# Kernel tuning notes

Measured on AMD Instinct MI355X. Metric: run time of the kernel, lower is better.

## Reference

```python
import jax, jax.numpy as jnp
import numpy as np

N, E = 20000, 160000
F, H, OUT = 256, 8, 128
L = 6            # total layers -> 5 GAT layers
LM1 = L - 1
NGN = L // 3 + 1 # 3 GraphNorms
D = F // H       # 32 per head
GN_FREQ = 3
EPS = 1e-5


def setup_inputs() -> dict:
    key = jax.random.key(0)
    ks = jax.random.split(key, 12)
    x = jax.random.normal(ks[0], (N, 1), dtype=jnp.float32)
    edge_index = jax.random.randint(ks[1], (2, E), 0, N, dtype=jnp.int32)
    W0 = jax.random.normal(ks[2], (1, F), dtype=jnp.float32) * 0.1
    b0 = jnp.zeros((F,), jnp.float32)
    gat_lin = jax.random.normal(ks[3], (LM1, F, F), dtype=jnp.float32) * (1.0 / np.sqrt(F))
    att_src = jax.random.normal(ks[4], (LM1, H, D), dtype=jnp.float32) * 0.1
    att_dst = jax.random.normal(ks[5], (LM1, H, D), dtype=jnp.float32) * 0.1
    gat_bias = jnp.zeros((LM1, F), jnp.float32)
    gn_weight = jnp.ones((NGN, F), jnp.float32)
    gn_bias = jnp.zeros((NGN, F), jnp.float32)
    gn_mean_scale = jnp.ones((NGN, F), jnp.float32)
    lin_W = jax.random.normal(ks[6], (F, OUT), dtype=jnp.float32) * (1.0 / np.sqrt(F))
    lin_b = jnp.zeros((OUT,), jnp.float32)
    return {"x": x, "W0": W0, "b0": b0, "gat_lin": gat_lin, "att_src": att_src,
            "att_dst": att_dst, "gat_bias": gat_bias, "gn_weight": gn_weight,
            "gn_bias": gn_bias, "gn_mean_scale": gn_mean_scale,
            "lin_W": lin_W, "lin_b": lin_b, "edge_index": edge_index}


def _gcn_conv(x, W, b, src, dst, n):
    h = x @ W
    deg = jax.ops.segment_sum(jnp.ones(src.shape[0], h.dtype), dst, num_segments=n)
    dinv = jnp.where(deg > 0, jax.lax.rsqrt(deg), 0.0)
    norm = dinv[src] * dinv[dst]                      # [E']
    out = jax.ops.segment_sum(h[src] * norm[:, None], dst, num_segments=n)
    return out + b


def _gat_conv(x, W, a_src, a_dst, src, dst, n):
    # PyG GATConv (concat=True, negative_slope=0.2, self-loops in src/dst)
    h = (x @ W).reshape(n, H, D)
    s = jnp.einsum('nhd,hd->nh', h, a_src)            # [N,H]
    t = jnp.einsum('nhd,hd->nh', h, a_dst)
    e = jax.nn.leaky_relu(s[src] + t[dst], 0.2)       # [E',H]
    m = jax.ops.segment_max(e, dst, num_segments=n)   # per-dst softmax
    e = jnp.exp(e - m[dst])
    denom = jax.ops.segment_sum(e, dst, num_segments=n)
    alpha = e / (denom[dst] + 1e-16)
    out = jax.ops.segment_sum(h[src] * alpha[:, :, None], dst, num_segments=n)
    return out.reshape(n, F)


def _graph_norm(x, w, b, ms):
    # PyG GraphNorm with batch=None (single graph): per-feature stats over nodes
    mean = jnp.mean(x, axis=0)
    out = x - ms * mean
    var = jnp.mean(out * out, axis=0)
    return w * out * jax.lax.rsqrt(var + EPS) + b


def reference(x, W0, b0, gat_lin, att_src, att_dst, gat_bias, gn_weight, gn_bias,
              gn_mean_scale, lin_W, lin_b, edge_index):
    n = x.shape[0]
    loops = jnp.arange(n, dtype=edge_index.dtype)
    src = jnp.concatenate([edge_index[0], loops])
    dst = jnp.concatenate([edge_index[1], loops])
    h = jax.nn.relu(_gcn_conv(x, W0, b0, src, dst, n))
    for i in range(LM1):
        if i % GN_FREQ == 0:
            g = i // GN_FREQ
            h = _graph_norm(h, gn_weight[g], gn_bias[g], gn_mean_scale[g])
        out = _gat_conv(h, gat_lin[i], att_src[i], att_dst[i], src, dst, n)
        if i % GN_FREQ == 0:
            out = out + gat_bias[i]
        h = h + jax.nn.relu(out)
    return h @ lin_W + lin_b
```

## Files before the change

kernel.cpp:

```cpp
#include <hip/hip_runtime.h>
#include <hip/hip_bf16.h>
#include <stdint.h>

typedef float f32x4 __attribute__((ext_vector_type(4)));
typedef short s16x8 __attribute__((ext_vector_type(8)));

__device__ __forceinline__ float bf2f(unsigned short u) {
    union { unsigned int i; float f; } v; v.i = ((unsigned int)u) << 16; return v.f;
}
__device__ __forceinline__ unsigned short f2bf(float f) {
    union { float f; unsigned int i; } v; v.f = f;
    unsigned int x = v.i;
    return (unsigned short)((x + 0x7fffu + ((x >> 16) & 1u)) >> 16);
}
__device__ __forceinline__ void bfp(unsigned int u, float& lo, float& hi) {
    union { unsigned int i; float f; } a, b;
    a.i = u << 16; b.i = u & 0xffff0000u;
    lo = a.f; hi = b.f;
}
__device__ __forceinline__ void gload16(const void* g, void* l) {
    __builtin_amdgcn_global_load_lds(
        (const __attribute__((address_space(1))) void*)g,
        (__attribute__((address_space(3))) void*)l, 16, 0, 0);
}

__global__ void k_prep(const int* __restrict__ ei, int E, int* __restrict__ deg,
                       int CB,
                       const float* __restrict__ gat_lin,
                       const float* __restrict__ lin_W,
                       const float* __restrict__ att_src,
                       const float* __restrict__ att_dst,
                       unsigned short* __restrict__ Wt,
                       unsigned short* __restrict__ lt) {
    int bid = blockIdx.x;
    if (bid < CB) {
        int e = bid * 256 + threadIdx.x;
        if (e < E) atomicAdd(&deg[ei[E + e]], 1);
        return;
    }
    int idx = (bid - CB) * 256 + threadIdx.x;
    const int T1 = 5 * 65536;
    const int T2 = T1 + 128 * 256;
    const int T3 = T2 + 5 * 64 * 256;
    if (idx < T1) {
        int l = idx >> 16, r = idx & 0xFFFF;
        int nrow = r >> 8, k = r & 255;
        Wt[(size_t)l * 81920 + nrow * 256 + k] =
            f2bf(gat_lin[(size_t)l * 65536 + k * 256 + nrow]);
    } else if (idx < T2) {
        int j = idx - T1;
        int nrow = j >> 8, k = j & 255;
        lt[nrow * 256 + k] = f2bf(lin_W[(size_t)k * 128 + nrow]);
    } else if (idx < T3) {
        int j = idx - T2;
        int l = j >> 14, r = j & 16383;
        int row = r >> 8, k = r & 255;
        float v = 0.f;
        if (row < 16) {
            int head = row & 7;
            const float* a = (row < 8) ? (att_src + l * 256 + head * 32)
                                       : (att_dst + l * 256 + head * 32);
            const float* wr = gat_lin + (size_t)l * 65536 + k * 256 + head * 32;
#pragma unroll
            for (int d = 0; d < 32; ++d) v += wr[d] * a[d];
        }
        Wt[(size_t)l * 81920 + (256 + row) * 256 + k] = f2bf(v);
    }
}

__global__ __launch_bounds__(256) void k_bsum(const int* __restrict__ deg,
                                              int* __restrict__ bsum, int n) {
    __shared__ int buf[256];
    int i = blockIdx.x * 256 + threadIdx.x;
    buf[threadIdx.x] = (i < n) ? deg[i] + 1 : 0;
    __syncthreads();
#pragma unroll
    for (int off = 128; off > 0; off >>= 1) {
        if ((int)threadIdx.x < off) buf[threadIdx.x] += buf[threadIdx.x + off];
        __syncthreads();
    }
    if (threadIdx.x == 0) bsum[blockIdx.x] = buf[0];
}

__global__ __launch_bounds__(256) void k_emit(const int* __restrict__ deg,
                                              const int* __restrict__ bsum,
                                              int* __restrict__ rowptr,
                                              int* __restrict__ wo,
                                              float* __restrict__ dinv, int n) {
    __shared__ int buf[256];
    int t = threadIdx.x;
    int bid = blockIdx.x;
    buf[t] = (t < bid) ? bsum[t] : 0;
    __syncthreads();
#pragma unroll
    for (int off = 128; off > 0; off >>= 1) {
        if (t < off) buf[t] += buf[t + off];
        __syncthreads();
    }
    int boff = buf[0];
    __syncthreads();
    int i = bid * 256 + t;
    int v = (i < n) ? deg[i] + 1 : 0;
    buf[t] = v;
    __syncthreads();
    for (int off = 1; off < 256; off <<= 1) {
        int add = (t >= off) ? buf[t - off] : 0;
        __syncthreads();
        buf[t] += add;
        __syncthreads();
    }
    if (i < n) {
        int excl = boff + buf[t] - v;
        rowptr[i] = excl;
        wo[i] = excl;
        dinv[i] = rsqrtf((float)v);
        if (i == n - 1) rowptr[n] = excl + v;
    }
}

__global__ void k_fill(const int* __restrict__ ei, int E, int n,
                       int* wo, int* srcs) {
    int e = blockIdx.x * blockDim.x + threadIdx.x;
    int EP = E + n;
    if (e >= EP) return;
    int s_, d_;
    if (e < E) { s_ = ei[e]; d_ = ei[E + e]; }
    else       { s_ = d_ = e - E; }
    int pos = atomicAdd(&wo[d_], 1);
    srcs[pos] = s_;
}

__global__ __launch_bounds__(256) void k_h0f(const float* __restrict__ x,
                                             const float* __restrict__ dinv,
                                             const int* __restrict__ rowptr,
                                             const int* __restrict__ srcs,
                                             const float* __restrict__ W0,
                                             const float* __restrict__ b0,
                                             unsigned short* __restrict__ hbf,
                                             int n, int Mpad) {
    int wave = threadIdx.x >> 6, lane = threadIdx.x & 63;
    int node = blockIdx.x * 4 + wave;
    if (node >= Mpad) return;
    size_t base = (size_t)node * 256 + lane * 4;
    if (node >= n) {
        ushort4 z = {0, 0, 0, 0};
        *reinterpret_cast<ushort4*>(hbf + base) = z;
        return;
    }
    int p0 = rowptr[node], p1 = rowptr[node + 1];
    float sum = 0.f;
    for (int p = p0 + lane; p < p1; p += 64) {
        int s = srcs[p];
        sum += x[s] * dinv[s];
    }
#pragma unroll
    for (int m = 1; m < 64; m <<= 1) sum += __shfl_xor(sum, m);
    float sv = sum * dinv[node];
    float4 wv = *reinterpret_cast<const float4*>(W0 + lane * 4);
    float4 bv = *reinterpret_cast<const float4*>(b0 + lane * 4);
    ushort4 o;
    o.x = f2bf(fmaxf(sv * wv.x + bv.x, 0.f));
    o.y = f2bf(fmaxf(sv * wv.y + bv.y, 0.f));
    o.z = f2bf(fmaxf(sv * wv.z + bv.z, 0.f));
    o.w = f2bf(fmaxf(sv * wv.w + bv.w, 0.f));
    *reinterpret_cast<ushort4*>(hbf + base) = o;
}

__global__ __launch_bounds__(256) void k_gn_reduce(const unsigned short* __restrict__ hbf,
                                                   float* sums, float* sumsq, int n) {
    int f = threadIdx.x;
    float s = 0.f, q = 0.f;
    for (int r = blockIdx.x; r < n; r += gridDim.x) {
        float v = bf2f(hbf[(size_t)r * 256 + f]);
        s += v; q += v * v;
    }
    atomicAdd(&sums[f], s);
    atomicAdd(&sumsq[f], q);
}

__global__ __launch_bounds__(256) void k_gnfold(const float* __restrict__ st,
                                                const float* __restrict__ w,
                                                const float* __restrict__ b,
                                                const float* __restrict__ ms,
                                                unsigned short* __restrict__ Wt,
                                                float* __restrict__ so,
                                                float* __restrict__ rowbias,
                                                float ninv) {
    __shared__ float red[256];
    int col = blockIdx.x, k = threadIdx.x;
    float mean = st[k] * ninv;
    float m2   = st[256 + k] * ninv;
    float msf  = ms[k];
    float var  = m2 + msf * mean * mean * (msf - 2.0f);
    float sc = w[k] * rsqrtf(var + 1e-5f);
    float of = b[k] - msf * mean * sc;
    size_t idx = (size_t)col * 256 + k;
    float wv = bf2f(Wt[idx]);
    red[k] = of * wv;
    __syncthreads();
#pragma unroll
    for (int off = 128; off > 0; off >>= 1) {
        if (k < off) red[k] += red[k + off];
        __syncthreads();
    }
    if (k == 0) rowbias[col] = red[0];
    Wt[idx] = f2bf(sc * wv);
    if (col == 0) { so[k] = sc; so[256 + k] = of; }
}

#define BM 64
__global__ __launch_bounds__(512) void k_gemm_mfma(
    const unsigned short* __restrict__ A,
    const unsigned short* __restrict__ Bt,
    unsigned short* __restrict__ Cb,
    float* __restrict__ Cf,
    float* __restrict__ sbuf,
    float* __restrict__ tbuf,
    const float* __restrict__ bias,
    const float* __restrict__ rowbias,
    int M, int ldc)
{
    __shared__ unsigned short As[64 * 256];
    __shared__ unsigned short Bs[64 * 256];
    const int tid = threadIdx.x;
    const int bm = blockIdx.x * BM;
    const int bn = blockIdx.y * 64;
    {
        const char* ga = (const char*)(A + (size_t)bm * 256);
        const char* gb = (const char*)(Bt + (size_t)bn * 256);
        char* la = (char*)As;
        char* lb = (char*)Bs;
#pragma unroll
        for (int i = 0; i < 4; ++i) {
            int o  = (i * 512 + tid) * 16;
            int so = o ^ (((o >> 9) & 7) << 4);
            gload16(ga + so, la + o);
            gload16(gb + so, lb + o);
        }
    }
    __syncthreads();

    const int lane = tid & 63;
    const int w  = tid >> 6;
    const int wm = (w >> 1) * 16;
    const int wn = (w & 1) * 32;
    const int r  = lane & 15, kb = lane >> 4;
    const int r4 = (lane >> 4) * 4, cc = lane & 15;
    const char* la = (const char*)As;
    const char* lb = (const char*)Bs;

    f32x4 acc[2] = {};
#pragma unroll
    for (int ks = 0; ks < 8; ++ks) {
        int row = wm + r;
        int c16 = (ks * 4 + kb) ^ (row & 7);
        s16x8 af = *(const s16x8*)(la + row * 512 + c16 * 16);
#pragma unroll
        for (int j = 0; j < 2; ++j) {
            int col = wn + j * 16 + r;
            int d16 = (ks * 4 + kb) ^ (col & 7);
            s16x8 bfr = *(const s16x8*)(lb + col * 512 + d16 * 16);
            acc[j] = __builtin_amdgcn_mfma_f32_16x16x32_bf16(af, bfr, acc[j], 0, 0, 0);
        }
    }
#pragma unroll
    for (int j = 0; j < 2; ++j) {
        int col = bn + wn + j * 16 + cc;
        float rb = rowbias ? rowbias[col] : 0.f;
#pragma unroll
        for (int q = 0; q < 4; ++q) {
            int row = bm + wm + r4 + q;
            float v = acc[j][q] + rb;
            if (Cb) {
                if (col < 256) {
                    Cb[(size_t)row * 256 + col] = f2bf(v);
                } else if (col < 264) {
                    sbuf[(size_t)row * 8 + (col - 256)] = v;
                } else if (col < 272) {
                    tbuf[(size_t)row * 8 + (col - 264)] = v;
                }
            } else if (row < M) {
                Cf[(size_t)row * ldc + col] = v + bias[col];
            }
        }
    }
}

__global__ __launch_bounds__(256) void k_fagg(const unsigned short* __restrict__ h1,
                                              const float* __restrict__ sbuf,
                                              const float* __restrict__ tbuf,
                                              const int* __restrict__ rowptr,
                                              const int* __restrict__ srcs,
                                              unsigned short* __restrict__ hbf,
                                              const float* __restrict__ bias,
                                              const float* __restrict__ so, int n) {
    int wave = threadIdx.x >> 6, lane = threadIdx.x & 63;
    int node = blockIdx.x * 4 + wave;
    if (node >= n) return;
    int p0 = rowptr[node], p1 = rowptr[node + 1];
    int hid = lane >> 5;
    int l5 = lane & 31;
    int fl = l5 * 8;
    int head = l5 >> 2;
    float tv = tbuf[node * 8 + head];
    float m = -1e30f, den = 0.f;
    float a0 = 0.f, a1 = 0.f, a2 = 0.f, a3 = 0.f;
    float a4 = 0.f, a5 = 0.f, a6 = 0.f, a7 = 0.f;
    int q = p0 + hid;
    for (; q + 6 < p1; q += 8) {
        int s0 = srcs[q], s1 = srcs[q + 2], s2 = srcs[q + 4], s3 = srcs[q + 6];
        float e0 = sbuf[s0 * 8 + head] + tv;
        float e1 = sbuf[s1 * 8 + head] + tv;
        float e2 = sbuf[s2 * 8 + head] + tv;
        float e3 = sbuf[s3 * 8 + head] + tv;
        uint4 v0 = *reinterpret_cast<const uint4*>(h1 + (size_t)s0 * 256 + fl);
        uint4 v1 = *reinterpret_cast<const uint4*>(h1 + (size_t)s1 * 256 + fl);
        uint4 v2 = *reinterpret_cast<const uint4*>(h1 + (size_t)s2 * 256 + fl);
        uint4 v3 = *reinterpret_cast<const uint4*>(h1 + (size_t)s3 * 256 + fl);
        e0 = (e0 > 0.f) ? e0 : 0.2f * e0;
        e1 = (e1 > 0.f) ? e1 : 0.2f * e1;
        e2 = (e2 > 0.f) ? e2 : 0.2f * e2;
        e3 = (e3 > 0.f) ? e3 : 0.2f * e3;
        float em = fmaxf(fmaxf(e0, e1), fmaxf(e2, e3));
        if (em > m + 8.f) {
            float sc = __expf(m - em);
            den *= sc;
            a0 *= sc; a1 *= sc; a2 *= sc; a3 *= sc;
            a4 *= sc; a5 *= sc; a6 *= sc; a7 *= sc;
            m = em;
        }
        float w0 = __expf(e0 - m), w1 = __expf(e1 - m);
        float w2 = __expf(e2 - m), w3 = __expf(e3 - m);
        den += (w0 + w1) + (w2 + w3);
        float fl0, fh0, fl1, fh1, fl2, fh2, fl3, fh3;
        bfp(v0.x, fl0, fh0); bfp(v1.x, fl1, fh1); bfp(v2.x, fl2, fh2); bfp(v3.x, fl3, fh3);
        a0 += (w0 * fl0 + w1 * fl1) + (w2 * fl2 + w3 * fl3);
        a1 += (w0 * fh0 + w1 * fh1) + (w2 * fh2 + w3 * fh3);
        bfp(v0.y, fl0, fh0); bfp(v1.y, fl1, fh1); bfp(v2.y, fl2, fh2); bfp(v3.y, fl3, fh3);
        a2 += (w0 * fl0 + w1 * fl1) + (w2 * fl2 + w3 * fl3);
        a3 += (w0 * fh0 + w1 * fh1) + (w2 * fh2 + w3 * fh3);
        bfp(v0.z, fl0, fh0); bfp(v1.z, fl1, fh1); bfp(v2.z, fl2, fh2); bfp(v3.z, fl3, fh3);
        a4 += (w0 * fl0 + w1 * fl1) + (w2 * fl2 + w3 * fl3);
        a5 += (w0 * fh0 + w1 * fh1) + (w2 * fh2 + w3 * fh3);
        bfp(v0.w, fl0, fh0); bfp(v1.w, fl1, fh1); bfp(v2.w, fl2, fh2); bfp(v3.w, fl3, fh3);
        a6 += (w0 * fl0 + w1 * fl1) + (w2 * fl2 + w3 * fl3);
        a7 += (w0 * fh0 + w1 * fh1) + (w2 * fh2 + w3 * fh3);
    }
    for (; q < p1; q += 2) {
        int s0 = srcs[q];
        float e0 = sbuf[s0 * 8 + head] + tv;
        uint4 v0 = *reinterpret_cast<const uint4*>(h1 + (size_t)s0 * 256 + fl);
        e0 = (e0 > 0.f) ? e0 : 0.2f * e0;
        if (e0 > m + 8.f) {
            float sc = __expf(m - e0);
            den *= sc;
            a0 *= sc; a1 *= sc; a2 *= sc; a3 *= sc;
            a4 *= sc; a5 *= sc; a6 *= sc; a7 *= sc;
            m = e0;
        }
        float w0 = __expf(e0 - m);
        den += w0;
        float f0l, f0h;
        bfp(v0.x, f0l, f0h); a0 += w0 * f0l; a1 += w0 * f0h;
        bfp(v0.y, f0l, f0h); a2 += w0 * f0l; a3 += w0 * f0h;
        bfp(v0.z, f0l, f0h); a4 += w0 * f0l; a5 += w0 * f0h;
        bfp(v0.w, f0l, f0h); a6 += w0 * f0l; a7 += w0 * f0h;
    }
    float mo = __shfl_xor(m, 32);
    float mm = fmaxf(m, mo);
    float sc = __expf(m - mm);
    den *= sc; den += __shfl_xor(den, 32);
    a0 *= sc; a0 += __shfl_xor(a0, 32);
    a1 *= sc; a1 += __shfl_xor(a1, 32);
    a2 *= sc; a2 += __shfl_xor(a2, 32);
    a3 *= sc; a3 += __shfl_xor(a3, 32);
    a4 *= sc; a4 += __shfl_xor(a4, 32);
    a5 *= sc; a5 += __shfl_xor(a5, 32);
    a6 *= sc; a6 += __shfl_xor(a6, 32);
    a7 *= sc; a7 += __shfl_xor(a7, 32);
    if (hid) return;
    float inv = 1.0f / (den + 1e-16f);
    a0 *= inv; a1 *= inv; a2 *= inv; a3 *= inv;
    a4 *= inv; a5 *= inv; a6 *= inv; a7 *= inv;
    float b_[8] = {0.f, 0.f, 0.f, 0.f, 0.f, 0.f, 0.f, 0.f};
    if (bias) {
        float4 blo = *reinterpret_cast<const float4*>(bias + fl);
        float4 bhi = *reinterpret_cast<const float4*>(bias + fl + 4);
        b_[0] = blo.x; b_[1] = blo.y; b_[2] = blo.z; b_[3] = blo.w;
        b_[4] = bhi.x; b_[5] = bhi.y; b_[6] = bhi.z; b_[7] = bhi.w;
    }
    size_t base = (size_t)node * 256 + fl;
    uint4 hv = *reinterpret_cast<const uint4*>(hbf + base);
    float h_[8];
    bfp(hv.x, h_[0], h_[1]); bfp(hv.y, h_[2], h_[3]);
    bfp(hv.z, h_[4], h_[5]); bfp(hv.w, h_[6], h_[7]);
    if (so) {
        float4 s0v = *reinterpret_cast<const float4*>(so + fl);
        float4 s1v = *reinterpret_cast<const float4*>(so + fl + 4);
        float4 o0v = *reinterpret_cast<const float4*>(so + 256 + fl);
        float4 o1v = *reinterpret_cast<const float4*>(so + 256 + fl + 4);
        h_[0] = h_[0] * s0v.x + o0v.x; h_[1] = h_[1] * s0v.y + o0v.y;
        h_[2] = h_[2] * s0v.z + o0v.z; h_[3] = h_[3] * s0v.w + o0v.w;
        h_[4] = h_[4] * s1v.x + o1v.x; h_[5] = h_[5] * s1v.y + o1v.y;
        h_[6] = h_[6] * s1v.z + o1v.z; h_[7] = h_[7] * s1v.w + o1v.w;
    }
    float r0 = h_[0] + fmaxf(a0 + b_[0], 0.f);
    float r1 = h_[1] + fmaxf(a1 + b_[1], 0.f);
    float r2 = h_[2] + fmaxf(a2 + b_[2], 0.f);
    float r3 = h_[3] + fmaxf(a3 + b_[3], 0.f);
    float r4 = h_[4] + fmaxf(a4 + b_[4], 0.f);
    float r5 = h_[5] + fmaxf(a5 + b_[5], 0.f);
    float r6 = h_[6] + fmaxf(a6 + b_[6], 0.f);
    float r7 = h_[7] + fmaxf(a7 + b_[7], 0.f);
    uint4 o;
    o.x = (unsigned int)f2bf(r0) | ((unsigned int)f2bf(r1) << 16);
    o.y = (unsigned int)f2bf(r2) | ((unsigned int)f2bf(r3) << 16);
    o.z = (unsigned int)f2bf(r4) | ((unsigned int)f2bf(r5) << 16);
    o.w = (unsigned int)f2bf(r6) | ((unsigned int)f2bf(r7) << 16);
    *reinterpret_cast<uint4*>(hbf + base) = o;
}

extern "C" void kernel_launch(void* const* d_in, const int* in_sizes, int n_in,
                              void* d_out, int out_size, void* d_ws, size_t ws_size,
                              hipStream_t stream) {
    const float* x        = (const float*)d_in[0];
    const float* W0       = (const float*)d_in[1];
    const float* b0       = (const float*)d_in[2];
    const float* gat_lin  = (const float*)d_in[3];
    const float* att_src  = (const float*)d_in[4];
    const float* att_dst  = (const float*)d_in[5];
    const float* gat_bias = (const float*)d_in[6];
    const float* gn_w     = (const float*)d_in[7];
    const float* gn_b     = (const float*)d_in[8];
    const float* gn_ms    = (const float*)d_in[9];
    const float* lin_W    = (const float*)d_in[10];
    const float* lin_b    = (const float*)d_in[11];
    const int*   ei       = (const int*)d_in[12];

    const int n  = in_sizes[0];
    const int E  = in_sizes[12] / 2;
    const int EP = E + n;
    const int Mpad = ((n + BM - 1) / BM) * BM;
    const int nb = (n + 255) / 256;

    char* w = (char*)d_ws;
    unsigned short* hbf = (unsigned short*)w; w += (size_t)Mpad * 256 * 2;
    unsigned short* h1  = (unsigned short*)w; w += (size_t)Mpad * 256 * 2;
    float* sbuf = (float*)w;                  w += (size_t)Mpad * 8 * 4;
    float* tbuf = (float*)w;                  w += (size_t)Mpad * 8 * 4;
    unsigned short* Wt = (unsigned short*)w;  w += (size_t)5 * 320 * 256 * 2;
    unsigned short* lt = (unsigned short*)w;  w += (size_t)128 * 256 * 2;
    float* scaleoff = (float*)w;              w += 1024 * 4;
    float* rowbias  = (float*)w;              w += 640 * 4;
    float* gnstat = (float*)w;                w += 1024 * 4;
    int* deg    = (int*)w;                    w += (size_t)n * 4;
    float* dinv = (float*)w;                  w += (size_t)n * 4;
    int* rowptr = (int*)w;                    w += ((size_t)(n + 1) * 4 + 15) / 16 * 16;
    int* wo     = (int*)w;                    w += (size_t)n * 4;
    int* bsum   = (int*)w;                    w += ((size_t)nb * 4 + 15) / 16 * 16;
    int* srcs   = (int*)w;                    w += (size_t)EP * 4;

    const int B256 = 256;
    auto cdiv = [](int a, int b) { return (a + b - 1) / b; };

    hipMemsetAsync(gnstat, 0, 1024 * 4 + (size_t)n * 4, stream);

    const int CB = cdiv(E, B256);
    const int WPREP = 5 * 65536 + 128 * 256 + 5 * 64 * 256;
    k_prep<<<CB + cdiv(WPREP, B256), B256, 0, stream>>>(
        ei, E, deg, CB, gat_lin, lin_W, att_src, att_dst, Wt, lt);

    k_bsum<<<nb, 256, 0, stream>>>(deg, bsum, n);
    k_emit<<<nb, 256, 0, stream>>>(deg, bsum, rowptr, wo, dinv, n);
    k_fill<<<cdiv(EP, B256), B256, 0, stream>>>(ei, E, n, wo, srcs);

    k_h0f<<<cdiv(Mpad, 4), 256, 0, stream>>>(x, dinv, rowptr, srcs, W0, b0, hbf, n, Mpad);

    const float ninv = 1.0f / (float)n;
    const int gx = Mpad / BM;

    for (int i = 0; i < 5; ++i) {
        const float* rb = nullptr;
        const float* so = nullptr;
        if (i % 3 == 0) {
            int g = i / 3;
            k_gn_reduce<<<256, 256, 0, stream>>>(hbf, gnstat + g * 512,
                                                 gnstat + g * 512 + 256, n);
            k_gnfold<<<320, 256, 0, stream>>>(gnstat + g * 512, gn_w + g * 256,
                                              gn_b + g * 256, gn_ms + g * 256,
                                              Wt + (size_t)i * 81920,
                                              scaleoff + g * 512, rowbias + g * 320, ninv);
            rb = rowbias + g * 320;
            so = scaleoff + g * 512;
        }
        k_gemm_mfma<<<dim3(gx, 5), 512, 0, stream>>>(
            hbf, Wt + (size_t)i * 81920, h1, nullptr, sbuf, tbuf, nullptr, rb,
            n, 256);
        k_fagg<<<cdiv(n, 4), 256, 0, stream>>>(
            h1, sbuf, tbuf, rowptr, srcs, hbf,
            (i % 3 == 0) ? gat_bias + i * 256 : nullptr, so, n);
    }

    k_gemm_mfma<<<dim3(gx, 2), 512, 0, stream>>>(
        hbf, lt, nullptr, (float*)d_out, nullptr, nullptr, lin_b, nullptr,
        n, 128);
}
```

Measured before the change: 281.4 us.

## Fuse GraphNorm reduce with weight fold, drop block-sum scan kernel, coalesce transposes

Merges the GraphNorm statistics reduction and the weight-folding kernel into one launch. The last block to finish, found with an atomic counter and threadfences, does the fold using wave shuffles. Removes the separate block-sum kernel by having each k_emit block sum all preceding degrees directly. Swaps the index mapping in the weight transpose so global reads are coalesced. This saves several kernel launches, at the cost of a serial fold in a single block and redundant degree reads in later emit blocks.

```diff
diff --git a/kernel.cpp b/kernel.cpp
--- a/kernel.cpp
+++ b/kernel.cpp
@@ -44,12 +44,12 @@
     const int T3 = T2 + 5 * 64 * 256;
     if (idx < T1) {
         int l = idx >> 16, r = idx & 0xFFFF;
-        int nrow = r >> 8, k = r & 255;
+        int k = r >> 8, nrow = r & 255;
         Wt[(size_t)l * 81920 + nrow * 256 + k] =
             f2bf(gat_lin[(size_t)l * 65536 + k * 256 + nrow]);
     } else if (idx < T2) {
         int j = idx - T1;
-        int nrow = j >> 8, k = j & 255;
+        int k = j >> 7, nrow = j & 127;
         lt[nrow * 256 + k] = f2bf(lin_W[(size_t)k * 128 + nrow]);
     } else if (idx < T3) {
         int j = idx - T2;
@@ -68,29 +68,17 @@
     }
 }
 
-__global__ __launch_bounds__(256) void k_bsum(const int* __restrict__ deg,
-                                              int* __restrict__ bsum, int n) {
-    __shared__ int buf[256];
-    int i = blockIdx.x * 256 + threadIdx.x;
-    buf[threadIdx.x] = (i < n) ? deg[i] + 1 : 0;
-    __syncthreads();
-#pragma unroll
-    for (int off = 128; off > 0; off >>= 1) {
-        if ((int)threadIdx.x < off) buf[threadIdx.x] += buf[threadIdx.x + off];
-        __syncthreads();
-    }
-    if (threadIdx.x == 0) bsum[blockIdx.x] = buf[0];
-}
-
 __global__ __launch_bounds__(256) void k_emit(const int* __restrict__ deg,
-                                              const int* __restrict__ bsum,
                                               int* __restrict__ rowptr,
                                               int* __restrict__ wo,
                                               float* __restrict__ dinv, int n) {
     __shared__ int buf[256];
     int t = threadIdx.x;
     int bid = blockIdx.x;
-    buf[t] = (t < bid) ? bsum[t] : 0;
+    int lim = bid * 256;
+    int s = 0;
+    for (int i = t; i < lim; i += 256) s += deg[i] + 1;
+    buf[t] = s;
     __syncthreads();
 #pragma unroll
     for (int off = 128; off > 0; off >>= 1) {
@@ -166,46 +154,53 @@
     *reinterpret_cast<ushort4*>(hbf + base) = o;
 }
 
-__global__ __launch_bounds__(256) void k_gn_reduce(const unsigned short* __restrict__ hbf,
-                                                   float* sums, float* sumsq, int n) {
+__global__ __launch_bounds__(256) void k_gn(const unsigned short* __restrict__ hbf,
+                                            float* __restrict__ st,
+                                            const float* __restrict__ w,
+                                            const float* __restrict__ b,
+                                            const float* __restrict__ ms,
+                                            unsigned short* __restrict__ Wt,
+                                            float* __restrict__ so,
+                                            float* __restrict__ rowbias,
+                                            int* __restrict__ cnt,
+                                            int n, float ninv) {
     int f = threadIdx.x;
     float s = 0.f, q = 0.f;
     for (int r = blockIdx.x; r < n; r += gridDim.x) {
         float v = bf2f(hbf[(size_t)r * 256 + f]);
         s += v; q += v * v;
     }
-    atomicAdd(&sums[f], s);
-    atomicAdd(&sumsq[f], q);
-}
-
-__global__ __launch_bounds__(256) void k_gnfold(const float* __restrict__ st,
-                                                const float* __restrict__ w,
-                                                const float* __restrict__ b,
-                                                const float* __restrict__ ms,
-                                                unsigned short* __restrict__ Wt,
-                                                float* __restrict__ so,
-                                                float* __restrict__ rowbias,
-                                                float ninv) {
-    __shared__ float red[256];
-    int col = blockIdx.x, k = threadIdx.x;
-    float mean = st[k] * ninv;
-    float m2   = st[256 + k] * ninv;
-    float msf  = ms[k];
-    float var  = m2 + msf * mean * mean * (msf - 2.0f);
-    float sc = w[k] * rsqrtf(var + 1e-5f);
-    float of = b[k] - msf * mean * sc;
-    size_t idx = (size_t)col * 256 + k;
-    float wv = bf2f(Wt[idx]);
-    red[k] = of * wv;
+    atomicAdd(&st[f], s);
+    atomicAdd(&st[256 + f], q);
+    __threadfence();
     __syncthreads();
-#pragma unroll
-    for (int off = 128; off > 0; off >>= 1) {
-        if (k < off) red[k] += red[k + off];
-        __syncthreads();
-    }
-    if (k == 0) rowbias[col] = red[0];
-    Wt[idx] = f2bf(sc * wv);
-    if (col == 0) { so[k] = sc; so[256 + k] = of; }
+    __shared__ int lastdone;
+    if (f == 0) lastdone = (atomicAdd(cnt, 1) == (int)gridDim.x - 1) ? 1 : 0;
+    __syncthreads();
+    if (!lastdone) return;
+    __threadfence();
+    int lane = f & 63, wv = f >> 6;
+    for (int col = wv; col < 320; col += 4) {
+        float partial = 0.f;
+#pragma unroll
+        for (int j = 0; j < 4; ++j) {
+            int k = lane * 4 + j;
+            float mean = st[k] * ninv;
+            float m2   = st[256 + k] * ninv;
+            float msf  = ms[k];
+            float var  = m2 + msf * mean * mean * (msf - 2.0f);
+            float sc = w[k] * rsqrtf(var + 1e-5f);
+            float of = b[k] - msf * mean * sc;
+            size_t idx = (size_t)col * 256 + k;
+            float wvv = bf2f(Wt[idx]);
+            partial += of * wvv;
+            Wt[idx] = f2bf(sc * wvv);
+            if (col == 0) { so[k] = sc; so[256 + k] = of; }
+        }
+#pragma unroll
+        for (int m = 1; m < 64; m <<= 1) partial += __shfl_xor(partial, m);
+        if (lane == 0) rowbias[col] = partial;
+    }
 }
 
 #define BM 64
@@ -453,25 +448,24 @@
     float* scaleoff = (float*)w;              w += 1024 * 4;
     float* rowbias  = (float*)w;              w += 640 * 4;
     float* gnstat = (float*)w;                w += 1024 * 4;
+    int* gncnt  = (int*)w;                    w += 16;
     int* deg    = (int*)w;                    w += (size_t)n * 4;
     float* dinv = (float*)w;                  w += (size_t)n * 4;
     int* rowptr = (int*)w;                    w += ((size_t)(n + 1) * 4 + 15) / 16 * 16;
     int* wo     = (int*)w;                    w += (size_t)n * 4;
-    int* bsum   = (int*)w;                    w += ((size_t)nb * 4 + 15) / 16 * 16;
     int* srcs   = (int*)w;                    w += (size_t)EP * 4;
 
     const int B256 = 256;
     auto cdiv = [](int a, int b) { return (a + b - 1) / b; };
 
-    hipMemsetAsync(gnstat, 0, 1024 * 4 + (size_t)n * 4, stream);
+    hipMemsetAsync(gnstat, 0, 1024 * 4 + 16 + (size_t)n * 4, stream);
 
     const int CB = cdiv(E, B256);
     const int WPREP = 5 * 65536 + 128 * 256 + 5 * 64 * 256;
     k_prep<<<CB + cdiv(WPREP, B256), B256, 0, stream>>>(
         ei, E, deg, CB, gat_lin, lin_W, att_src, att_dst, Wt, lt);
 
-    k_bsum<<<nb, 256, 0, stream>>>(deg, bsum, n);
-    k_emit<<<nb, 256, 0, stream>>>(deg, bsum, rowptr, wo, dinv, n);
+    k_emit<<<nb, 256, 0, stream>>>(deg, rowptr, wo, dinv, n);
     k_fill<<<cdiv(EP, B256), B256, 0, stream>>>(ei, E, n, wo, srcs);
 
     k_h0f<<<cdiv(Mpad, 4), 256, 0, stream>>>(x, dinv, rowptr, srcs, W0, b0, hbf, n, Mpad);
@@ -484,12 +478,12 @@
         const float* so = nullptr;
         if (i % 3 == 0) {
             int g = i / 3;
-            k_gn_reduce<<<256, 256, 0, stream>>>(hbf, gnstat + g * 512,
-                                                 gnstat + g * 512 + 256, n);
-            k_gnfold<<<320, 256, 0, stream>>>(gnstat + g * 512, gn_w + g * 256,
-                                              gn_b + g * 256, gn_ms + g * 256,
-                                              Wt + (size_t)i * 81920,
-                                              scaleoff + g * 512, rowbias + g * 320, ninv);
+            k_gn<<<256, 256, 0, stream>>>(hbf, gnstat + g * 512,
+                                          gn_w + g * 256, gn_b + g * 256,
+                                          gn_ms + g * 256,
+                                          Wt + (size_t)i * 81920,
+                                          scaleoff + g * 512, rowbias + g * 320,
+                                          gncnt + g, n, ninv);
             rb = rowbias + g * 320;
             so = scaleoff + g * 512;
         }
```

After: 457.9 us. 62.7% more time.
